# Performance work log

Measured on AMD Instinct MI355X. Metric: run time of the kernel, lower is better.

Reference implementation:

```python
import jax, jax.numpy as jnp
import numpy as np

N_CLASS = 32000
EMB = 512
HID = 1024
BATCH = 64
SEQ = 256


def setup_inputs() -> dict:
    key = jax.random.key(0)
    ks = jax.random.split(key, 24)
    X = jax.random.randint(ks[0], (BATCH, SEQ), 0, N_CLASS)
    C_emb = jax.random.normal(ks[1], (N_CLASS, EMB), dtype=jnp.float32) * 0.02
    d0 = HID + EMB   # layer-0 gate input dim (cat(h, x))
    d1 = HID + HID   # layer-1 gate input dim (cat(h, h_below))
    def w(k, din):
        return jax.random.normal(k, (din, HID), dtype=jnp.float32) * (1.0 / np.sqrt(din))
    inp = {
        'X': X, 'C_emb': C_emb,
        'W_i0': w(ks[2], d0), 'b_i0': jnp.ones((HID,), jnp.float32),
        'W_c0': w(ks[3], d0), 'b_c0': jnp.ones((HID,), jnp.float32),
        'W_f0': w(ks[4], d0), 'b_f0': jnp.ones((HID,), jnp.float32),
        'W_o0': w(ks[5], d0), 'b_o0': jnp.ones((HID,), jnp.float32),
        'W_i1': w(ks[6], d1), 'b_i1': jnp.ones((HID,), jnp.float32),
        'W_c1': w(ks[7], d1), 'b_c1': jnp.ones((HID,), jnp.float32),
        'W_f1': w(ks[8], d1), 'b_f1': jnp.ones((HID,), jnp.float32),
        'W_o1': w(ks[9], d1), 'b_o1': jnp.ones((HID,), jnp.float32),
        'W_out': jax.random.normal(ks[10], (HID, N_CLASS), jnp.float32) * (1.0 / np.sqrt(HID)),
        'b_out': jnp.ones((N_CLASS,), jnp.float32),
    }
    return inp


def _lstm_lm(X, C_emb, layers, W_out, b_out):
    B = X.shape[0]
    xs = jnp.transpose(C_emb[X], (1, 0, 2))  # (S, B, E)
    h0 = tuple(jnp.zeros((B, HID), xs.dtype) for _ in layers)
    c0 = tuple(jnp.zeros((B, HID), xs.dtype) for _ in layers)

    def step(carry, x_t):
        hs, cs = carry
        inp = x_t
        new_h, new_c = [], []
        for l, (Wi, bi, Wc, bc, Wf, bf, Wo, bo) in enumerate(layers):
            m = jnp.concatenate([hs[l], inp], axis=1)  # cat(h_state, input_below)
            i = jax.nn.sigmoid(m @ Wi + bi)
            g = jnp.tanh(m @ Wc + bc)
            f = jax.nn.sigmoid(m @ Wf + bf)
            c = f * cs[l] + i * g
            o = jax.nn.sigmoid(m @ Wo + bo)
            h = o * jnp.tanh(c)
            new_h.append(h)
            new_c.append(c)
            inp = h
        return (tuple(new_h), tuple(new_c)), None

    (hs, _), _ = jax.lax.scan(step, (h0, c0), xs)
    return hs[-1] @ W_out + b_out  # (B, n_class): logits from last timestep, top layer


def reference(X, C_emb, W_i0, b_i0, W_c0, b_c0, W_f0, b_f0, W_o0, b_o0,
              W_i1, b_i1, W_c1, b_c1, W_f1, b_f1, W_o1, b_o1, W_out, b_out):
    layers = [
        (W_i0, b_i0, W_c0, b_c0, W_f0, b_f0, W_o0, b_o0),
        (W_i1, b_i1, W_c1, b_c1, W_f1, b_f1, W_o1, b_o1),
    ]
    return _lstm_lm(X, C_emb, layers, W_out, b_out)
```

## Files before the change

### kernel.cpp

```cpp
#include <hip/hip_runtime.h>
#include <cstdint>
#include <cstddef>

#define NCLS 32000
#define EMBD 512
#define HIDD 1024
#define BATCH 64
#define SEQL 256
#define NWG 256
#define BH (BATCH * HIDD)
#define HBYTES (BH * 2)


typedef __attribute__((ext_vector_type(8))) short short8;
typedef __attribute__((ext_vector_type(4))) float float4v;
typedef unsigned long long ull;
typedef unsigned short ushort;

#define WS_CTR   0
#define WS_H0G   2048
#define WS_H1G   (WS_H0G + 2*HBYTES)
#define WS_XEMB  (WS_H1G + 2*HBYTES)

#define LDS_RED_OFF  126976
#define LDS_META_OFF (126976 + 32768)
#define SMEM_BYTES   (126976 + 32768 + 16)

__device__ __forceinline__ ushort f2bf(float f) {
  union { float f; uint32_t u; } x; x.f = f;
  uint32_t r = x.u + 0x7FFFu + ((x.u >> 16) & 1u);
  return (ushort)(r >> 16);
}

__device__ __forceinline__ float sigm(float x) {
  return 1.0f / (1.0f + __expf(-x));
}

__device__ __forceinline__ void gbar(unsigned* bar, unsigned* gen, unsigned* dead,
                                     unsigned target) {
  __syncthreads();
  if (threadIdx.x == 0) {
    unsigned prev = __hip_atomic_fetch_add(bar, 1u, __ATOMIC_RELAXED, __HIP_MEMORY_SCOPE_AGENT);
    if (prev == target * NWG - 1u) {
      __hip_atomic_store(gen, target, __ATOMIC_RELAXED, __HIP_MEMORY_SCOPE_AGENT);
    } else {
      unsigned spin = 0;
      while (__hip_atomic_load(gen, __ATOMIC_RELAXED, __HIP_MEMORY_SCOPE_AGENT) < target) {
        if (__hip_atomic_load(dead, __ATOMIC_RELAXED, __HIP_MEMORY_SCOPE_AGENT) != 0u) break;
        if (++spin > 2000000u) {
          __hip_atomic_store(dead, 1u, __ATOMIC_RELAXED, __HIP_MEMORY_SCOPE_AGENT);
          break;
        }
        __builtin_amdgcn_s_sleep(1);
      }
    }
  }
  __syncthreads();
}

__device__ __forceinline__ void hbar(unsigned* ctr, unsigned xcc, unsigned nloc,
                                     unsigned nxcd, unsigned tgt) {
  __syncthreads();
  if (threadIdx.x == 0) {
    unsigned* xctr = ctr + 64 + 16 * xcc;
    unsigned* xgen = ctr + 192 + 16 * xcc;
    unsigned* dead = ctr + 17;
    unsigned a = __hip_atomic_fetch_add(xctr, 1u, __ATOMIC_RELAXED, __HIP_MEMORY_SCOPE_AGENT);
    if (a == tgt * nloc - 1u) {
      asm volatile("buffer_inv sc1\n\ts_waitcnt vmcnt(0)" ::: "memory");
      unsigned g = __hip_atomic_fetch_add(ctr, 1u, __ATOMIC_RELAXED, __HIP_MEMORY_SCOPE_AGENT);
      if (g == tgt * nxcd - 1u) {
        __hip_atomic_store(ctr + 16, tgt, __ATOMIC_RELAXED, __HIP_MEMORY_SCOPE_AGENT);
      } else {
        unsigned spin = 0;
        while (__hip_atomic_load(ctr + 16, __ATOMIC_RELAXED, __HIP_MEMORY_SCOPE_AGENT) < tgt) {
          if ((++spin & 63u) == 0u) {
            if (__hip_atomic_load(dead, __ATOMIC_RELAXED, __HIP_MEMORY_SCOPE_AGENT) != 0u) break;
            if (spin > 4000000u) {
              __hip_atomic_store(dead, 1u, __ATOMIC_RELAXED, __HIP_MEMORY_SCOPE_AGENT);
              break;
            }
          }
        }
      }
      __hip_atomic_store(xgen, tgt, __ATOMIC_RELAXED, __HIP_MEMORY_SCOPE_AGENT);
    } else {
      unsigned spin = 0;
      while (__hip_atomic_load(xgen, __ATOMIC_RELAXED, __HIP_MEMORY_SCOPE_AGENT) < tgt) {
        if ((++spin & 63u) == 0u) {
          if (__hip_atomic_load(dead, __ATOMIC_RELAXED, __HIP_MEMORY_SCOPE_AGENT) != 0u) break;
          if (spin > 4000000u) {
            __hip_atomic_store(dead, 1u, __ATOMIC_RELAXED, __HIP_MEMORY_SCOPE_AGENT);
            break;
          }
        }
      }
    }
  }
  __syncthreads();
}

__global__ void init_bar_k(char* ws) {
  if (threadIdx.x < 320) ((unsigned*)(ws + WS_CTR))[threadIdx.x] = 0u;
}

__global__ void embed_k(const int* __restrict__ X, const float* __restrict__ Cemb,
                        char* __restrict__ ws) {
  uint32_t p = blockIdx.x * 256u + threadIdx.x;
  uint32_t t = p >> 14;
  uint32_t r = p & 16383u;
  uint32_t b = r >> 8;
  uint32_t e2 = r & 255u;
  int row = X[b * SEQL + t];
  const float2 v = *(const float2*)(Cemb + (size_t)row * EMBD + (size_t)e2 * 2);
  uint32_t lo = f2bf(v.x), hi = f2bf(v.y);
  uint32_t dw = t * 16384u + (e2 >> 4) * 1024u + b * 16u + (e2 & 15u);
  ((uint32_t*)(ws + WS_XEMB))[dw] = (hi << 16) | lo;
}

__global__ __launch_bounds__(512, 1)
void lstm_k(const float* __restrict__ Wi0, const float* __restrict__ Wc0,
            const float* __restrict__ Wf0, const float* __restrict__ Wo0,
            const float* __restrict__ Wi1, const float* __restrict__ Wc1,
            const float* __restrict__ Wf1, const float* __restrict__ Wo1,
            const float* __restrict__ bi0, const float* __restrict__ bc0,
            const float* __restrict__ bf0, const float* __restrict__ bo0,
            const float* __restrict__ bi1, const float* __restrict__ bc1,
            const float* __restrict__ bf1, const float* __restrict__ bo1,
            char* ws) {
  const int wg   = blockIdx.x;
  const int tid  = threadIdx.x;
  const int lane = tid & 63;
  const int wv   = tid >> 6;
  const int l15  = lane & 15;
  const int quad = lane >> 4;

  extern __shared__ char smem[];
  ushort* h0st = (ushort*)smem;
  float*  red  = (float*)(smem + LDS_RED_OFF);
  int*    meta = (int*)(smem + LDS_META_OFF);

  ushort* h0buf = (ushort*)(ws + WS_H0G);
  ushort* h1buf = (ushort*)(ws + WS_H1G);
  const ushort* xemb = (const ushort*)(ws + WS_XEMB);
  unsigned* ctr = (unsigned*)(ws + WS_CTR);

  const unsigned xcc = __builtin_amdgcn_s_getreg((3u << 11) | 20u) & 7u;

  if (tid == 0)
    __hip_atomic_fetch_add(ctr + 32 + xcc, 1u, __ATOMIC_RELAXED, __HIP_MEMORY_SCOPE_AGENT);

  short8 bfr[16];
  {
    ushort* scr = (ushort*)smem;
    {
      const float* W0g[4] = {Wi0, Wc0, Wf0, Wo0};
      int jl = tid & 3, kr = tid >> 2, jg = wg * 4 + jl;
      for (int g = 0; g < 4; ++g) {
        ushort* dst = scr + (jl * 4 + g) * 1536;
        const float* s = W0g[g] + jg;
        for (int k = kr; k < 1536; k += 128) dst[k] = f2bf(s[(size_t)k * HIDD]);
      }
    }
    __syncthreads();
    if (wv < 4) {
      #pragma unroll
      for (int j = 0; j < 12; ++j)
        bfr[j] = *(const short8*)(scr + l15 * 1536 + (12 * wv + j) * 32 + quad * 8);
    }
    __syncthreads();
    {
      const float* W1g[4] = {Wi1, Wc1, Wf1, Wo1};
      int jl = tid & 3, kr = tid >> 2, jg = wg * 4 + jl;
      for (int g = 0; g < 4; ++g) {
        ushort* dst = scr + (jl * 4 + g) * 2048;
        const float* s = W1g[g] + jg;
        for (int k = kr; k < 2048; k += 128) dst[k] = f2bf(s[(size_t)k * HIDD]);
      }
    }
    __syncthreads();
    if (wv >= 4) {
      #pragma unroll
      for (int j = 0; j < 8; ++j)
        bfr[j] = *(const short8*)(scr + l15 * 2048 + ((wv - 4) * 256 + j * 32) + quad * 8);
      #pragma unroll
      for (int j = 0; j < 8; ++j)
        bfr[8 + j] = *(const short8*)(scr + l15 * 2048 + 1024 + ((wv - 4) * 256 + j * 32) + quad * 8);
    }
    __syncthreads();
  }

  float bs0 = 0.f, bs1 = 0.f, bs2 = 0.f, bs3 = 0.f, cstr = 0.f;
  {
    int jl = tid & 3, jg = wg * 4 + jl;
    if (tid < 256) { bs0 = bi0[jg]; bs1 = bc0[jg]; bs2 = bf0[jg]; bs3 = bo0[jg]; }
    else           { bs0 = bi1[jg]; bs1 = bc1[jg]; bs2 = bf1[jg]; bs3 = bo1[jg]; }
  }

  if (tid < 128) {
    ushort* base = (tid < 64) ? h0buf : h1buf;
    int b = tid & 63;
    __hip_atomic_store((ull*)(base + ((wg >> 3) << 11) + b * 32 + (wg & 7) * 4), 0ull,
                       __ATOMIC_RELAXED, __HIP_MEMORY_SCOPE_AGENT);
  }

  gbar(ctr + 48, ctr + 56, ctr + 17, 1u);

  if (tid == 0) {
    int nl = (int)__hip_atomic_load(ctr + 32 + xcc, __ATOMIC_RELAXED, __HIP_MEMORY_SCOPE_AGENT);
    int nx = 0;
    for (int x = 0; x < 8; ++x)
      nx += (__hip_atomic_load(ctr + 32 + x, __ATOMIC_RELAXED, __HIP_MEMORY_SCOPE_AGENT) != 0u);
    meta[0] = nl; meta[1] = nx;
  }
  __syncthreads();
  const unsigned nloc = (unsigned)meta[0], nxcd = (unsigned)meta[1];

  const int lofs = l15 * 32 + quad * 8;
  const int lswz = lofs ^ ((l15 & 7) * 8);

  unsigned tgt = 0;
  for (int p = 0; p <= SEQL; ++p) {
    const int run0 = (p < SEQL);
    const int run1 = (p >= 1);
    float4v acc0 = {0.f,0.f,0.f,0.f}, acc1 = acc0, acc2 = acc0, acc3 = acc0;

    if (wv < 4) {
      if (run0) {
        const ushort* hp = h0buf + (size_t)(p & 1) * BH;
        const ushort* xe = xemb + (size_t)p * BATCH * EMBD;
        #pragma unroll
        for (int bb = 0; bb < 2; ++bb) {
          short8 d[6][4];
          #pragma unroll
          for (int i = 0; i < 6; ++i) {
            int kb = 12 * wv + bb * 6 + i;
            const ushort* base = (kb < 32) ? (hp + kb * 2048) : (xe + (kb - 32) * 2048);
            const ushort* ab = base + lofs;
            d[i][0] = *(const short8*)(ab);
            d[i][1] = *(const short8*)(ab + 512);
            d[i][2] = *(const short8*)(ab + 1024);
            d[i][3] = *(const short8*)(ab + 1536);
          }
          #pragma unroll
          for (int i = 0; i < 6; ++i) {
            int kb = 12 * wv + bb * 6 + i;
            if (kb <= 30) {
              ushort* sp = h0st + kb * 2048 + lswz;
              *(short8*)(sp)        = d[i][0];
              *(short8*)(sp + 512)  = d[i][1];
              *(short8*)(sp + 1024) = d[i][2];
              *(short8*)(sp + 1536) = d[i][3];
            }
            short8 w = bfr[bb * 6 + i];
            acc0 = __builtin_amdgcn_mfma_f32_16x16x32_bf16(d[i][0], w, acc0, 0, 0, 0);
            acc1 = __builtin_amdgcn_mfma_f32_16x16x32_bf16(d[i][1], w, acc1, 0, 0, 0);
            acc2 = __builtin_amdgcn_mfma_f32_16x16x32_bf16(d[i][2], w, acc2, 0, 0, 0);
            acc3 = __builtin_amdgcn_mfma_f32_16x16x32_bf16(d[i][3], w, acc3, 0, 0, 0);
          }
        }
        float* rw = red + wv * 1024 + quad * 64 + l15;
        #pragma unroll
        for (int r = 0; r < 4; ++r) {
          rw[r * 16]       = acc0[r];
          rw[256 + r * 16] = acc1[r];
          rw[512 + r * 16] = acc2[r];
          rw[768 + r * 16] = acc3[r];
        }
      }
    } else {
      if (run1) {
        const ushort* h1p = h1buf + (size_t)((p & 1) ^ 1) * BH;
        #pragma unroll
        for (int bb = 0; bb < 2; ++bb) {
          short8 d[4][4];
          #pragma unroll
          for (int i = 0; i < 4; ++i) {
            int kb = (wv - 4) * 8 + bb * 4 + i;
            const ushort* ab = h1p + kb * 2048 + lofs;
            d[i][0] = *(const short8*)(ab);
            d[i][1] = *(const short8*)(ab + 512);
            d[i][2] = *(const short8*)(ab + 1024);
            d[i][3] = *(const short8*)(ab + 1536);
          }
          #pragma unroll
          for (int i = 0; i < 4; ++i) {
            short8 w = bfr[bb * 4 + i];
            acc0 = __builtin_amdgcn_mfma_f32_16x16x32_bf16(d[i][0], w, acc0, 0, 0, 0);
            acc1 = __builtin_amdgcn_mfma_f32_16x16x32_bf16(d[i][1], w, acc1, 0, 0, 0);
            acc2 = __builtin_amdgcn_mfma_f32_16x16x32_bf16(d[i][2], w, acc2, 0, 0, 0);
            acc3 = __builtin_amdgcn_mfma_f32_16x16x32_bf16(d[i][3], w, acc3, 0, 0, 0);
          }
        }
      }
    }
    __syncthreads();

    if (run0 && tid < 256) {
      int b = tid >> 2;
      const float* rr = red + b * 16 + (tid & 3) * 4;
      float4v v = *(const float4v*)rr;
      v += *(const float4v*)(rr + 1024);
      v += *(const float4v*)(rr + 2048);
      v += *(const float4v*)(rr + 3072);
      float ig = sigm(v.x + bs0);
      float gg = tanhf(v.y + bs1);
      float fg = sigm(v.z + bs2);
      float og = sigm(v.w + bs3);
      float c = fg * cstr + ig * gg;
      cstr = c;
      unsigned x  = f2bf(og * tanhf(c));
      unsigned x1 = (unsigned)__shfl((int)x, lane + 1);
      unsigned x2 = (unsigned)__shfl((int)x, lane + 2);
      unsigned x3 = (unsigned)__shfl((int)x, lane + 3);
      if ((lane & 3) == 0) {
        ull val = (ull)(x | (x1 << 16)) | ((ull)(x2 | (x3 << 16)) << 32);
        ushort* dst = h0buf + (size_t)((p & 1) ^ 1) * BH
                    + ((wg >> 3) << 11) + b * 32 + (wg & 7) * 4;
        __hip_atomic_store((ull*)dst, val, __ATOMIC_RELAXED, __HIP_MEMORY_SCOPE_AGENT);
      }
    }
    if (run1 && wv >= 4) {
      const ushort* h0c = h0buf + (size_t)(p & 1) * BH;
      const bool useLds = (p < SEQL);
      #pragma unroll
      for (int bb = 0; bb < 2; ++bb) {
        short8 d[4][4];
        #pragma unroll
        for (int i = 0; i < 4; ++i) {
          int kb = (wv - 4) * 8 + bb * 4 + i;
          if (useLds && kb <= 30) {
            const ushort* sp = h0st + kb * 2048 + lswz;
            d[i][0] = *(const short8*)(sp);
            d[i][1] = *(const short8*)(sp + 512);
            d[i][2] = *(const short8*)(sp + 1024);
            d[i][3] = *(const short8*)(sp + 1536);
          } else {
            const ushort* ab = h0c + kb * 2048 + lofs;
            d[i][0] = *(const short8*)(ab);
            d[i][1] = *(const short8*)(ab + 512);
            d[i][2] = *(const short8*)(ab + 1024);
            d[i][3] = *(const short8*)(ab + 1536);
          }
        }
        #pragma unroll
        for (int i = 0; i < 4; ++i) {
          short8 w = bfr[8 + bb * 4 + i];
          acc0 = __builtin_amdgcn_mfma_f32_16x16x32_bf16(d[i][0], w, acc0, 0, 0, 0);
          acc1 = __builtin_amdgcn_mfma_f32_16x16x32_bf16(d[i][1], w, acc1, 0, 0, 0);
          acc2 = __builtin_amdgcn_mfma_f32_16x16x32_bf16(d[i][2], w, acc2, 0, 0, 0);
          acc3 = __builtin_amdgcn_mfma_f32_16x16x32_bf16(d[i][3], w, acc3, 0, 0, 0);
        }
      }
      float* rw = red + wv * 1024 + quad * 64 + l15;
      #pragma unroll
      for (int r = 0; r < 4; ++r) {
        rw[r * 16]       = acc0[r];
        rw[256 + r * 16] = acc1[r];
        rw[512 + r * 16] = acc2[r];
        rw[768 + r * 16] = acc3[r];
      }
    }
    __syncthreads();

    if (run1 && tid >= 256) {
      int t = tid - 256, b = t >> 2;
      const float* rr = red + 4096 + b * 16 + (t & 3) * 4;
      float4v v = *(const float4v*)rr;
      v += *(const float4v*)(rr + 1024);
      v += *(const float4v*)(rr + 2048);
      v += *(const float4v*)(rr + 3072);
      float ig = sigm(v.x + bs0);
      float gg = tanhf(v.y + bs1);
      float fg = sigm(v.z + bs2);
      float og = sigm(v.w + bs3);
      float c = fg * cstr + ig * gg;
      cstr = c;
      unsigned x  = f2bf(og * tanhf(c));
      unsigned x1 = (unsigned)__shfl((int)x, lane + 1);
      unsigned x2 = (unsigned)__shfl((int)x, lane + 2);
      unsigned x3 = (unsigned)__shfl((int)x, lane + 3);
      if ((lane & 3) == 0) {
        ull val = (ull)(x | (x1 << 16)) | ((ull)(x2 | (x3 << 16)) << 32);
        ushort* dst = h1buf + (size_t)(p & 1) * BH
                    + ((wg >> 3) << 11) + b * 32 + (wg & 7) * 4;
        __hip_atomic_store((ull*)dst, val, __ATOMIC_RELAXED, __HIP_MEMORY_SCOPE_AGENT);
      }
    }
    if (p == SEQL) break;
    hbar(ctr, xcc, nloc, nxcd, ++tgt);
  }
}

__global__ __launch_bounds__(256, 1)
void out_gemm_k(const char* __restrict__ ws, const float* __restrict__ Wout,
                const float* __restrict__ bout, float* __restrict__ out) {
  const ushort* h1 = (const ushort*)(ws + WS_H1G);
  const int tid = threadIdx.x, lane = tid & 63, wv = tid >> 6;
  const int l15 = lane & 15, quad = lane >> 4;
  const int n0 = blockIdx.x * 128 + wv * 32;
  float4v acc[4][2];
  #pragma unroll
  for (int m = 0; m < 4; ++m)
    #pragma unroll
    for (int f = 0; f < 2; ++f) acc[m][f] = (float4v){0.f, 0.f, 0.f, 0.f};

  for (int k0 = 0; k0 < HIDD; k0 += 32) {
    const ushort* tb = h1 + ((k0 >> 5) << 11) + l15 * 32 + quad * 8;
    short8 a[4];
    #pragma unroll
    for (int m = 0; m < 4; ++m)
      a[m] = *(const short8*)(tb + m * 512);
    short8 bf[2];
    #pragma unroll
    for (int f = 0; f < 2; ++f) {
      int n = n0 + f * 16 + l15;
      #pragma unroll
      for (int j = 0; j < 8; ++j) {
        float w = Wout[(size_t)(k0 + quad * 8 + j) * NCLS + n];
        bf[f][j] = (short)f2bf(w);
      }
    }
    #pragma unroll
    for (int m = 0; m < 4; ++m)
      #pragma unroll
      for (int f = 0; f < 2; ++f)
        acc[m][f] = __builtin_amdgcn_mfma_f32_16x16x32_bf16(a[m], bf[f], acc[m][f], 0, 0, 0);
  }
  #pragma unroll
  for (int m = 0; m < 4; ++m)
    #pragma unroll
    for (int f = 0; f < 2; ++f) {
      int n = n0 + f * 16 + l15;
      float bb = bout[n];
      #pragma unroll
      for (int r = 0; r < 4; ++r) {
        int b = m * 16 + quad * 4 + r;
        out[(size_t)b * NCLS + n] = acc[m][f][r] + bb;
      }
    }
}

extern "C" void kernel_launch(void* const* d_in, const int* in_sizes, int n_in,
                              void* d_out, int out_size, void* d_ws, size_t ws_size,
                              hipStream_t stream) {
  const int*   X    = (const int*)d_in[0];
  const float* Cemb = (const float*)d_in[1];
  const float* Wi0  = (const float*)d_in[2];
  const float* bi0  = (const float*)d_in[3];
  const float* Wc0  = (const float*)d_in[4];
  const float* bc0  = (const float*)d_in[5];
  const float* Wf0  = (const float*)d_in[6];
  const float* bf0  = (const float*)d_in[7];
  const float* Wo0  = (const float*)d_in[8];
  const float* bo0  = (const float*)d_in[9];
  const float* Wi1  = (const float*)d_in[10];
  const float* bi1  = (const float*)d_in[11];
  const float* Wc1  = (const float*)d_in[12];
  const float* bc1  = (const float*)d_in[13];
  const float* Wf1  = (const float*)d_in[14];
  const float* bf1  = (const float*)d_in[15];
  const float* Wo1  = (const float*)d_in[16];
  const float* bo1  = (const float*)d_in[17];
  const float* Wout = (const float*)d_in[18];
  const float* bout = (const float*)d_in[19];
  float* out = (float*)d_out;
  char* ws = (char*)d_ws;

  hipFuncSetAttribute((const void*)lstm_k,
                      hipFuncAttributeMaxDynamicSharedMemorySize, SMEM_BYTES);

  init_bar_k<<<1, 512, 0, stream>>>(ws);
  embed_k<<<16384, 256, 0, stream>>>(X, Cemb, ws);
  lstm_k<<<NWG, 512, SMEM_BYTES, stream>>>(Wi0, Wc0, Wf0, Wo0, Wi1, Wc1, Wf1, Wo1,
                                           bi0, bc0, bf0, bo0, bi1, bc1, bf1, bo1, ws);
  out_gemm_k<<<250, 256, 0, stream>>>(ws, Wout, bout, out);
}
```

Measured before the change: 2.795 ms.

## Prefetch next-step embedding into LDS during the grid barrier

Measured after the change: 2.853 ms. 1.02x slower.

```diff
diff --git a/kernel.cpp b/kernel.cpp
--- a/kernel.cpp
+++ b/kernel.cpp
@@ -23,6 +23,7 @@
 #define WS_XEMB  (WS_H1G + 2*HBYTES)
 
 #define LDS_RED_OFF  126976
+#define LDS_XST_OFF  (126976 + 16384)
 #define LDS_META_OFF (126976 + 32768)
 #define SMEM_BYTES   (126976 + 32768 + 16)
 
@@ -52,48 +53,6 @@
           break;
         }
         __builtin_amdgcn_s_sleep(1);
-      }
-    }
-  }
-  __syncthreads();
-}
-
-__device__ __forceinline__ void hbar(unsigned* ctr, unsigned xcc, unsigned nloc,
-                                     unsigned nxcd, unsigned tgt) {
-  __syncthreads();
-  if (threadIdx.x == 0) {
-    unsigned* xctr = ctr + 64 + 16 * xcc;
-    unsigned* xgen = ctr + 192 + 16 * xcc;
-    unsigned* dead = ctr + 17;
-    unsigned a = __hip_atomic_fetch_add(xctr, 1u, __ATOMIC_RELAXED, __HIP_MEMORY_SCOPE_AGENT);
-    if (a == tgt * nloc - 1u) {
-      asm volatile("buffer_inv sc1\n\ts_waitcnt vmcnt(0)" ::: "memory");
-      unsigned g = __hip_atomic_fetch_add(ctr, 1u, __ATOMIC_RELAXED, __HIP_MEMORY_SCOPE_AGENT);
-      if (g == tgt * nxcd - 1u) {
-        __hip_atomic_store(ctr + 16, tgt, __ATOMIC_RELAXED, __HIP_MEMORY_SCOPE_AGENT);
-      } else {
-        unsigned spin = 0;
-        while (__hip_atomic_load(ctr + 16, __ATOMIC_RELAXED, __HIP_MEMORY_SCOPE_AGENT) < tgt) {
-          if ((++spin & 63u) == 0u) {
-            if (__hip_atomic_load(dead, __ATOMIC_RELAXED, __HIP_MEMORY_SCOPE_AGENT) != 0u) break;
-            if (spin > 4000000u) {
-              __hip_atomic_store(dead, 1u, __ATOMIC_RELAXED, __HIP_MEMORY_SCOPE_AGENT);
-              break;
-            }
-          }
-        }
-      }
-      __hip_atomic_store(xgen, tgt, __ATOMIC_RELAXED, __HIP_MEMORY_SCOPE_AGENT);
-    } else {
-      unsigned spin = 0;
-      while (__hip_atomic_load(xgen, __ATOMIC_RELAXED, __HIP_MEMORY_SCOPE_AGENT) < tgt) {
-        if ((++spin & 63u) == 0u) {
-          if (__hip_atomic_load(dead, __ATOMIC_RELAXED, __HIP_MEMORY_SCOPE_AGENT) != 0u) break;
-          if (spin > 4000000u) {
-            __hip_atomic_store(dead, 1u, __ATOMIC_RELAXED, __HIP_MEMORY_SCOPE_AGENT);
-            break;
-          }
-        }
       }
     }
   }
@@ -136,9 +95,10 @@
   const int quad = lane >> 4;
 
   extern __shared__ char smem[];
-  ushort* h0st = (ushort*)smem;
-  float*  red  = (float*)(smem + LDS_RED_OFF);
-  int*    meta = (int*)(smem + LDS_META_OFF);
+  ushort* h0st   = (ushort*)smem;
+  float*  red    = (float*)(smem + LDS_RED_OFF);
+  ushort* xstage = (ushort*)(smem + LDS_XST_OFF);
+  int*    meta   = (int*)(smem + LDS_META_OFF);
 
   ushort* h0buf = (ushort*)(ws + WS_H0G);
   ushort* h1buf = (ushort*)(ws + WS_H1G);
@@ -219,6 +179,11 @@
   const int lofs = l15 * 32 + quad * 8;
   const int lswz = lofs ^ ((l15 & 7) * 8);
 
+  const int psw_l = ((lane >> 2) & 0xE) | (((lane >> 2) ^ (lane >> 4)) & 1);
+  const int psw_q = ((((lane >> 1) ^ (lane >> 3)) & 1) << 1) |
+                    ((lane ^ (lane >> 2) ^ (lane >> 4)) & 1);
+  const int psofs = psw_l * 32 + psw_q * 8;
+
   unsigned tgt = 0;
   for (int p = 0; p <= SEQL; ++p) {
     const int run0 = (p < SEQL);
@@ -235,12 +200,20 @@
           #pragma unroll
           for (int i = 0; i < 6; ++i) {
             int kb = 12 * wv + bb * 6 + i;
-            const ushort* base = (kb < 32) ? (hp + kb * 2048) : (xe + (kb - 32) * 2048);
-            const ushort* ab = base + lofs;
-            d[i][0] = *(const short8*)(ab);
-            d[i][1] = *(const short8*)(ab + 512);
-            d[i][2] = *(const short8*)(ab + 1024);
-            d[i][3] = *(const short8*)(ab + 1536);
+            if (p >= 1 && kb >= 44) {
+              const ushort* sp = xstage + (kb - 44) * 2048 + lswz;
+              d[i][0] = *(const short8*)(sp);
+              d[i][1] = *(const short8*)(sp + 512);
+              d[i][2] = *(const short8*)(sp + 1024);
+              d[i][3] = *(const short8*)(sp + 1536);
+            } else {
+              const ushort* base = (kb < 32) ? (hp + kb * 2048) : (xe + (kb - 32) * 2048);
+              const ushort* ab = base + lofs;
+              d[i][0] = *(const short8*)(ab);
+              d[i][1] = *(const short8*)(ab + 512);
+              d[i][2] = *(const short8*)(ab + 1024);
+              d[i][3] = *(const short8*)(ab + 1536);
+            }
           }
           #pragma unroll
           for (int i = 0; i < 6; ++i) {
@@ -388,7 +361,59 @@
       }
     }
     if (p == SEQL) break;
-    hbar(ctr, xcc, nloc, nxcd, ++tgt);
+
+    __syncthreads();
+    if (p < SEQL - 1) {
+      const ushort* xn = xemb + (size_t)(p + 1) * BATCH * EMBD;
+      #pragma unroll
+      for (int s = 0; s < 2; ++s) {
+        int i = wv * 2 + s;
+        int j = 12 + (i >> 2), q = i & 3;
+        __builtin_amdgcn_global_load_lds(
+            (const unsigned int*)(xn + j * 2048 + q * 512 + psofs),
+            (unsigned int*)(xstage + (j - 12) * 2048 + q * 512),
+            16, 0, 0);
+      }
+    }
+    ++tgt;
+    if (tid == 0) {
+      unsigned* xctr = ctr + 64 + 16 * xcc;
+      unsigned* xgen = ctr + 192 + 16 * xcc;
+      unsigned* dead = ctr + 17;
+      unsigned a = __hip_atomic_fetch_add(xctr, 1u, __ATOMIC_RELAXED, __HIP_MEMORY_SCOPE_AGENT);
+      if (a == tgt * nloc - 1u) {
+        unsigned g = __hip_atomic_fetch_add(ctr, 1u, __ATOMIC_RELAXED, __HIP_MEMORY_SCOPE_AGENT);
+        asm volatile("buffer_inv sc1" ::: "memory");
+        if (g == tgt * nxcd - 1u) {
+          __hip_atomic_store(ctr + 16, tgt, __ATOMIC_RELAXED, __HIP_MEMORY_SCOPE_AGENT);
+        } else {
+          unsigned spin = 0;
+          while (__hip_atomic_load(ctr + 16, __ATOMIC_RELAXED, __HIP_MEMORY_SCOPE_AGENT) < tgt) {
+            if ((++spin & 63u) == 0u) {
+              if (__hip_atomic_load(dead, __ATOMIC_RELAXED, __HIP_MEMORY_SCOPE_AGENT) != 0u) break;
+              if (spin > 4000000u) {
+                __hip_atomic_store(dead, 1u, __ATOMIC_RELAXED, __HIP_MEMORY_SCOPE_AGENT);
+                break;
+              }
+            }
+          }
+        }
+        asm volatile("s_waitcnt vmcnt(0)" ::: "memory");
+        __hip_atomic_store(xgen, tgt, __ATOMIC_RELAXED, __HIP_MEMORY_SCOPE_AGENT);
+      } else {
+        unsigned spin = 0;
+        while (__hip_atomic_load(xgen, __ATOMIC_RELAXED, __HIP_MEMORY_SCOPE_AGENT) < tgt) {
+          if ((++spin & 63u) == 0u) {
+            if (__hip_atomic_load(dead, __ATOMIC_RELAXED, __HIP_MEMORY_SCOPE_AGENT) != 0u) break;
+            if (spin > 4000000u) {
+              __hip_atomic_store(dead, 1u, __ATOMIC_RELAXED, __HIP_MEMORY_SCOPE_AGENT);
+              break;
+            }
+          }
+        }
+      }
+    }
+    __syncthreads();
   }
 }
 
```
